# Optimization experiments

Measured on AMD Instinct MI355X. Metric: run time of the kernel, lower is better.

## Reference

```python
import jax, jax.numpy as jnp
import numpy as np

B, T, D = 8, 2048, 512
S = 4                 # n_slots
SLOT_DIM = D          # cfg.slot_dim defaults to d_model
SE = 8                # state_embed_dim
GH = 64               # gate_hidden
EMA = 0.99
SIGMA_FLOOR = 1e-3
OPEN2CLOSING, CLOSING2LOCKED, UNLOCK = 0.1, 0.03, 0.25
GAINS = jnp.array([1.0, 0.5, 0.1], dtype=jnp.float32)  # OPEN, CLOSING, LOCKED


def _glorot(k, shape, fi, fo):
    b = (6.0 / (fi + fo)) ** 0.5
    return jax.random.uniform(k, shape, jnp.float32, -b, b)


def setup_inputs() -> dict:
    key = jax.random.key(0)
    ks = jax.random.split(key, 8)
    gate_in = D + 1 + SE  # [h, z, state_embed]
    return {
        'h_seq': jax.random.normal(ks[0], (B, T, D), jnp.float32),
        'pred_W': _glorot(ks[1], (S, D, D), D, D),
        'pred_b': jnp.zeros((S, D), jnp.float32),
        'gate_W1': _glorot(ks[2], (S, gate_in, GH), gate_in, GH),
        'gate_b1': jnp.zeros((S, GH), jnp.float32),
        'gate_W2': _glorot(ks[3], (S, GH, 1), GH, 1),
        'gate_b2': jnp.zeros((S, 1), jnp.float32),
        'write_W': _glorot(ks[4], (S, D, SLOT_DIM), D, SLOT_DIM),
        'write_b': jnp.zeros((S, SLOT_DIM), jnp.float32),
        'w0': jnp.zeros((S, SLOT_DIM), jnp.float32),
        'state_embed': jax.random.normal(ks[5], (3, SE), jnp.float32),
    }


def reference(h_seq, pred_W, pred_b, gate_W1, gate_b1, gate_W2, gate_b2,
              write_W, write_b, w0, state_embed):
    Bb, Tt, Dd = h_seq.shape
    h_det = jax.lax.stop_gradient(h_seq)
    # per-slot next-step predictions (input detached, as in torch): (B,T,S,D)
    preds = jnp.einsum('btd,sdo->btso', h_det, pred_W) + pred_b
    # prediction emitted at t-1 targets h_t
    pred_prev = jnp.concatenate([jnp.zeros_like(preds[:, :1]), preds[:, :-1]], axis=1)
    valid = jnp.arange(Tt) > 0  # no surprise signal at t=0

    m0 = jnp.broadcast_to(w0, (Bb, S, SLOT_DIM)).astype(h_seq.dtype)
    carry0 = (m0,
              jnp.zeros((S,), jnp.float32),       # mu
              jnp.ones((S,), jnp.float32),        # sigma
              jnp.full((S,), 0.5, jnp.float32),   # gate_ema
              jnp.zeros((S,), jnp.int32))         # slot_state

    def step(carry, xs):
        m, mu, sigma, gate_ema, state = carry
        h_t, p_prev, ok = xs  # (B,D), (B,S,D), scalar bool
        # prediction-error surprise per slot
        err = jnp.sqrt(jnp.sum((p_prev - h_t[:, None, :]) ** 2, axis=-1) + 1e-8)  # (B,S)
        err = jnp.where(ok, err, 0.0)
        z = (err - mu) / jnp.maximum(sigma, SIGMA_FLOOR)  # (B,S)
        # gate MLP over [h, z, state_embed]
        se = state_embed[state]  # (S,SE)
        gin = jnp.concatenate([
            jnp.broadcast_to(h_t[:, None, :], (Bb, S, Dd)),
            z[..., None],
            jnp.broadcast_to(se[None], (Bb, S, SE))], axis=-1)
        hid = jax.nn.relu(jnp.einsum('bsi,sih->bsh', gin, gate_W1) + gate_b1)
        g = jax.nn.sigmoid(jnp.einsum('bsh,sho->bso', hid, gate_W2) + gate_b2)[..., 0]  # (B,S)
        # state-dependent write gain (OPEN/CLOSING/LOCKED)
        g_eff = g * GAINS[state]
        w_enc = jnp.einsum('bd,sdo->bso', h_t, write_W) + write_b
        m = (1.0 - g_eff[..., None]) * m + g_eff[..., None] * w_enc
        read = m.reshape(Bb, S * SLOT_DIM)
        # homeostatic bookkeeping (buffers: non-differentiable, EMA)
        err_s = jax.lax.stop_gradient(err)
        mu_n = jnp.where(ok, EMA * mu + (1 - EMA) * err_s.mean(0), mu)
        sigma_n = jnp.where(ok, EMA * sigma + (1 - EMA) * jnp.abs(err_s - mu).mean(0), sigma)
        gate_ema_n = EMA * gate_ema + (1 - EMA) * jax.lax.stop_gradient(g).mean(0)
        # state machine transitions on gate EMA
        st = jnp.where((state == 0) & (gate_ema_n < OPEN2CLOSING), 1, state)
        st = jnp.where((state == 1) & (gate_ema_n < CLOSING2LOCKED), 2,
             jnp.where((state == 1) & (gate_ema_n > UNLOCK), 0, st))
        st = jnp.where((state == 2) & (gate_ema_n > UNLOCK), 0, st)
        return (m, mu_n, sigma_n, gate_ema_n, st), read

    xs = (jnp.swapaxes(h_seq, 0, 1), jnp.swapaxes(pred_prev, 0, 1), valid)
    _, reads = jax.lax.scan(step, carry0, xs)
    return jnp.swapaxes(reads, 0, 1)  # (B,T,S*SLOT_DIM)
```

## Files before the change

### kernel.cpp

```cpp
#include <hip/hip_runtime.h>
#include <hip/hip_bf16.h>

#define Bb 8
#define Tt 2048
#define Dd 512
#define Ss 4
#define GHh 64
#define NCHUNK 64
#define CH 32

typedef __hip_bfloat16 bf16;
typedef short bf16x8 __attribute__((ext_vector_type(8)));
typedef float f32x4 __attribute__((ext_vector_type(4)));
__device__ __forceinline__ float b2f(bf16 x){ return __bfloat162float(x); }

#define GLOAD_LDS16(g, l) \
  __builtin_amdgcn_global_load_lds((const __attribute__((address_space(1))) unsigned int*)(const void*)(g), \
                                   (__attribute__((address_space(3))) unsigned int*)(l), 16, 0, 0)

__global__ __launch_bounds__(256) void k0a_cvt(const float* __restrict__ h, bf16* __restrict__ hb){
  int i = (blockIdx.x*256 + threadIdx.x)*4;
  float4 v = *reinterpret_cast<const float4*>(&h[i]);
  hb[i+0] = __float2bfloat16(v.x);
  hb[i+1] = __float2bfloat16(v.y);
  hb[i+2] = __float2bfloat16(v.z);
  hb[i+3] = __float2bfloat16(v.w);
}

__global__ __launch_bounds__(256) void k0b_pack(const float* __restrict__ predW,
    const float* __restrict__ writeW, const float* __restrict__ gateW1, bf16* __restrict__ Wt){
  __shared__ float tile[32][33];
  int k0 = blockIdx.x*32, n0 = blockIdx.y*32;
  int tx = threadIdx.x & 31, ty = threadIdx.x >> 5;
  #pragma unroll
  for (int p = 0; p < 4; ++p) {
    int kk = ty + p*8;
    int n = n0 + tx, k = k0 + kk;
    float v;
    if (n < 2048)      { int s=n>>9, o=n&511;              v = predW[((size_t)s*512+k)*512+o]; }
    else if (n < 4096) { int n2=n-2048; int s=n2>>9,o=n2&511; v = writeW[((size_t)s*512+k)*512+o]; }
    else               { int n2=n-4096; int s=n2>>6,hh=n2&63; v = gateW1[((size_t)s*521+k)*64+hh]; }
    tile[kk][tx] = v;
  }
  __syncthreads();
  #pragma unroll
  for (int p = 0; p < 4; ++p) {
    int nn = ty + p*8;
    Wt[(size_t)(n0+nn)*512 + k0 + tx] = __float2bfloat16(tile[tx][nn]);
  }
}

__global__ __launch_bounds__(256) void k1_mfma(
    const bf16* __restrict__ hb, const bf16* __restrict__ Wt,
    const float* __restrict__ h, const float* __restrict__ predb, const float* __restrict__ writeb,
    bf16* __restrict__ wenc, float* __restrict__ hg, float* __restrict__ errsq)
{
  __shared__ bf16 As[2][128*64];
  __shared__ bf16 Bs[2][128*64];
  const int tid = threadIdx.x;
  const int w = tid >> 6, lane = tid & 63;
  const int n0 = blockIdx.x * 128;
  const int row0 = blockIdx.y * 128;
  const int wm = w & 1, wn = w >> 1;
  const int mrow = lane & 15, kq = lane >> 4;

  f32x4 acc[4][4];
  #pragma unroll
  for (int i=0;i<4;++i)
    #pragma unroll
    for (int j=0;j<4;++j) acc[i][j] = (f32x4){0.f,0.f,0.f,0.f};

  const int srow  = lane >> 3;
  const int sslot = (lane & 7) ^ srow;
  const bf16* gaBase = hb + (size_t)(row0 + w*32 + srow)*512 + sslot*8;
  const bf16* gbBase = Wt + (size_t)(n0  + w*32 + srow)*512 + sslot*8;

  auto STAGE = [&](int buf, int kstep){
    const bf16* ga = gaBase + kstep*64;
    const bf16* gb = gbBase + kstep*64;
    bf16* lA = &As[buf][(w*32)*64];
    bf16* lB = &Bs[buf][(w*32)*64];
    #pragma unroll
    for (int i=0;i<4;++i) {
      GLOAD_LDS16(ga + (size_t)i*8*512, lA + i*8*64);
      GLOAD_LDS16(gb + (size_t)i*8*512, lB + i*8*64);
    }
  };

  auto COMPUTE = [&](int buf){
    #pragma unroll
    for (int kk=0; kk<2; ++kk) {
      bf16x8 af[4], bfr[4];
      #pragma unroll
      for (int mi=0;mi<4;++mi) {
        int r = wm*64 + mi*16 + mrow;
        af[mi] = *reinterpret_cast<const bf16x8*>(&As[buf][r*64 + (((kk*4+kq) ^ (r&7))<<3)]);
      }
      #pragma unroll
      for (int ni=0;ni<4;++ni) {
        int r = wn*64 + ni*16 + mrow;
        bfr[ni] = *reinterpret_cast<const bf16x8*>(&Bs[buf][r*64 + (((kk*4+kq) ^ (r&7))<<3)]);
      }
      #pragma unroll
      for (int mi=0;mi<4;++mi)
        #pragma unroll
        for (int ni=0;ni<4;++ni)
          acc[mi][ni] = __builtin_amdgcn_mfma_f32_16x16x32_bf16(af[mi], bfr[ni], acc[mi][ni], 0, 0, 0);
    }
  };

  STAGE(0, 0);
  __syncthreads();
  #pragma unroll
  for (int t = 0; t < 8; ++t) {
    if (t < 7) STAGE((t+1)&1, t+1);
    COMPUTE(t&1);
    __syncthreads();
  }

  if (n0 < 2048) {
    const int s = n0 >> 9;
    #pragma unroll
    for (int mi=0;mi<4;++mi) {
      #pragma unroll
      for (int reg=0;reg<4;++reg) {
        int r = row0 + wm*64 + mi*16 + kq*4 + reg;
        float sum = 0.f;
        if ((r & 2047) != 2047) {
          #pragma unroll
          for (int ni=0;ni<4;++ni) {
            int o = (n0 & 511) + wn*64 + ni*16 + mrow;
            float P = acc[mi][ni][reg] + predb[s*512 + o];
            float d = P - h[(size_t)(r+1)*512 + o];
            sum = fmaf(d, d, sum);
          }
        }
        #pragma unroll
        for (int off=1; off<16; off<<=1) sum += __shfl_xor(sum, off);
        if (mrow == 0 && (r & 2047) != 2047)
          atomicAdd(&errsq[(size_t)(r+1)*4 + s], sum);
      }
    }
  } else if (n0 < 4096) {
    #pragma unroll
    for (int mi=0;mi<4;++mi)
      #pragma unroll
      for (int ni=0;ni<4;++ni) {
        int n2 = n0 - 2048 + wn*64 + ni*16 + mrow;
        int s = n2 >> 9, o = n2 & 511;
        float wb = writeb[s*512 + o];
        #pragma unroll
        for (int reg=0;reg<4;++reg) {
          int r = row0 + wm*64 + mi*16 + kq*4 + reg;
          wenc[((size_t)r*4 + s)*512 + o] = __float2bfloat16(acc[mi][ni][reg] + wb);
        }
      }
  } else {
    #pragma unroll
    for (int mi=0;mi<4;++mi)
      #pragma unroll
      for (int ni=0;ni<4;++ni) {
        int n2 = n0 - 4096 + wn*64 + ni*16 + mrow;
        int s = n2 >> 6, hh = n2 & 63;
        #pragma unroll
        for (int reg=0;reg<4;++reg) {
          int r = row0 + wm*64 + mi*16 + kq*4 + reg;
          hg[((size_t)r*4 + s)*64 + hh] = acc[mi][ni][reg];
        }
      }
  }
}

__global__ void k2a_err(const float* __restrict__ errsq, float* __restrict__ err){
  int i = blockIdx.x*256 + threadIdx.x;
  int t = (i >> 2) & 2047;
  err[i] = (t > 0) ? sqrtf(errsq[i] + 1e-8f) : 0.f;
}

__global__ void k2b_em(const float* __restrict__ err, float* __restrict__ em){
  int i = blockIdx.x*256 + threadIdx.x;
  float sum = 0.f;
  #pragma unroll
  for (int b=0;b<8;++b) sum += err[b*8192 + i];
  em[i] = sum * 0.125f;
}

__global__ __launch_bounds__(256) void k2c_scan(const float* __restrict__ in, float* __restrict__ outv, float init){
  __shared__ float s_in[8192];
  __shared__ float sA[256], sB[256], s_entry[256];
  for (int i = threadIdx.x; i < 8192; i += 256) s_in[i] = in[i];
  __syncthreads();
  const int c = threadIdx.x >> 2, s = threadIdx.x & 3;
  float A = 1.f, B = 0.f;
  #pragma unroll 8
  for (int i = 0; i < 32; ++i) {
    int t = c*32 + i;
    if (t >= 1) { A *= 0.99f; B = fmaf(0.99f, B, 0.01f * s_in[t*4 + s]); }
  }
  sA[threadIdx.x] = A; sB[threadIdx.x] = B;
  __syncthreads();
  if (threadIdx.x < 4) {
    int ss = threadIdx.x;
    float v = init;
    for (int cc = 0; cc < 64; ++cc) {
      s_entry[cc*4 + ss] = v;
      v = fmaf(sA[cc*4 + ss], v, sB[cc*4 + ss]);
    }
  }
  __syncthreads();
  float v = s_entry[threadIdx.x];
  #pragma unroll 8
  for (int i = 0; i < 32; ++i) {
    int t = c*32 + i;
    outv[t*4 + s] = v;
    if (t >= 1) v = fmaf(0.99f, v, 0.01f * s_in[t*4 + s]);
  }
}

__global__ void k2d_sd(const float* __restrict__ err, const float* __restrict__ MU, float* __restrict__ sd){
  int i = blockIdx.x*256 + threadIdx.x;
  float mu = MU[i];
  float sum = 0.f;
  #pragma unroll
  for (int b=0;b<8;++b) sum += fabsf(err[b*8192 + i] - mu);
  sd[i] = sum * 0.125f;
}

__global__ void k2e_base(const float* __restrict__ gateW1, const float* __restrict__ semb,
                         const float* __restrict__ gateb1, float* __restrict__ base1){
  int i = blockIdx.x*256 + threadIdx.x;
  if (i < 768) {
    int hh = i & 63, k = (i >> 6) % 3, s = i / 192;
    float acc = gateb1[s*64 + hh];
    #pragma unroll
    for (int e = 0; e < 8; ++e)
      acc = fmaf(semb[k*8+e], gateW1[((size_t)s*521 + 513 + e)*64 + hh], acc);
    base1[i] = acc;
  }
}

__global__ void k3_gall(const float* __restrict__ hg, const float* __restrict__ err,
    const float* __restrict__ MU, const float* __restrict__ SIG,
    const float* __restrict__ gateW1, const float* __restrict__ base1,
    const float* __restrict__ gateW2, const float* __restrict__ gateb2,
    float* __restrict__ g_all)
{
  int i = blockIdx.x*256 + threadIdx.x;
  int k = i % 3;
  int bts = i / 3;
  int s = bts & 3;
  int t = (bts >> 2) & 2047;
  float e = err[bts];
  float z = (e - MU[t*4+s]) / fmaxf(SIG[t*4+s], 1e-3f);
  const float* hgp = &hg[(size_t)bts*64];
  const float* b1p = &base1[(s*3 + k)*64];
  const float* w1zp = &gateW1[((size_t)s*521 + 512)*64];
  const float* w2p = &gateW2[s*64];
  float logit = 0.f;
  for (int hh = 0; hh < 64; ++hh) {
    float hid = hgp[hh] + z*w1zp[hh] + b1p[hh];
    hid = fmaxf(hid, 0.f);
    logit = fmaf(hid, w2p[hh], logit);
  }
  logit += gateb2[s];
  g_all[i] = 1.f/(1.f + expf(-logit));
}

__global__ void k3b_gm(const float* __restrict__ g_all, float* __restrict__ gm){
  int i = blockIdx.x*256 + threadIdx.x;
  float sum = 0.f;
  #pragma unroll
  for (int b=0;b<8;++b) sum += g_all[((size_t)b*8192 + i/3)*3 + (i%3)];
  gm[i] = sum * 0.125f;
}

__global__ __launch_bounds__(256) void k4_scan(const float* __restrict__ gm, int* __restrict__ states){
  __shared__ float s_gm[2][6144];
  for (int i = threadIdx.x; i < 6144; i += 256) s_gm[0][i] = gm[i];
  __syncthreads();
  float ema = 0.5f; int st = 0;
  for (int c = 0; c < 4; ++c) {
    if (c < 3)
      for (int i = threadIdx.x; i < 6144; i += 256) s_gm[(c+1)&1][i] = gm[(c+1)*6144 + i];
    if (threadIdx.x < 4) {
      int s = threadIdx.x;
      const float* gp = &s_gm[c&1][s*3];
      int* sp = &states[c*2048 + s];
      #pragma unroll 8
      for (int tt = 0; tt < 512; ++tt) {
        sp[tt*4] = st;
        float g0 = gp[tt*12+0], g1 = gp[tt*12+1], g2 = gp[tt*12+2];
        float base = 0.99f * ema;
        float e0 = fmaf(0.01f, g0, base);
        float e1 = fmaf(0.01f, g1, base);
        float e2 = fmaf(0.01f, g2, base);
        ema = (st == 0) ? e0 : ((st == 1) ? e1 : e2);
        int n0 = (ema < 0.1f) ? 1 : 0;
        int n1 = (ema < 0.03f) ? 2 : ((ema > 0.25f) ? 0 : 1);
        int n2 = (ema > 0.25f) ? 0 : 2;
        st = (st == 0) ? n0 : ((st == 1) ? n1 : n2);
      }
    }
    __syncthreads();
  }
}

__global__ void k5_a(const float* __restrict__ g_all, const int* __restrict__ states, float* __restrict__ a){
  int i = blockIdx.x*256 + threadIdx.x;
  int ts = i & 8191;
  int st = states[ts];
  float gain = (st == 0) ? 1.f : ((st == 1) ? 0.5f : 0.1f);
  a[i] = g_all[(size_t)i*3 + st] * gain;
}

__global__ __launch_bounds__(64) void k6_pass1(const float* __restrict__ a, const bf16* __restrict__ wenc,
      float* __restrict__ q, float* __restrict__ Pc){
  int c = blockIdx.x, s = blockIdx.y, b = blockIdx.z;
  int d0 = threadIdx.x << 3;
  __shared__ float s_a[CH];
  if (threadIdx.x < CH) s_a[threadIdx.x] = a[(size_t)(b*2048 + c*CH + threadIdx.x)*4 + s];
  __syncthreads();
  float qv[8];
  #pragma unroll
  for (int j=0;j<8;++j) qv[j] = 0.f;
  float p = 1.f;
  const bf16* wp = &wenc[((size_t)(b*2048 + c*CH)*4 + s)*512 + d0];
  #pragma unroll 4
  for (int i = 0; i < CH; ++i) {
    float av = s_a[i];
    bf16x8 wv = *reinterpret_cast<const bf16x8*>(wp + (size_t)i*4*512);
    float om = 1.f - av;
    #pragma unroll
    for (int j=0;j<8;++j) qv[j] = fmaf(om, qv[j], av*b2f(((const bf16*)&wv)[j]));
    p *= om;
  }
  float* qp = &q[((size_t)(b*4+s)*NCHUNK + c)*512 + d0];
  #pragma unroll
  for (int j=0;j<8;++j) qp[j] = qv[j];
  if (threadIdx.x == 0) Pc[(b*4+s)*NCHUNK + c] = p;
}

__global__ __launch_bounds__(512) void k7_bound(const float* __restrict__ q, const float* __restrict__ Pc,
      const float* __restrict__ w0, float* __restrict__ m_start){
  int s = blockIdx.x, b = blockIdx.y, d = threadIdx.x;
  float m = w0[s*512 + d];
  for (int c = 0; c < NCHUNK; ++c) {
    m_start[((size_t)(b*4+s)*NCHUNK + c)*512 + d] = m;
    m = Pc[(b*4+s)*NCHUNK + c]*m + q[((size_t)(b*4+s)*NCHUNK + c)*512 + d];
  }
}

__global__ __launch_bounds__(64) void k8_pass2(const float* __restrict__ a, const bf16* __restrict__ wenc,
      const float* __restrict__ m_start, float* __restrict__ out){
  int c = blockIdx.x, s = blockIdx.y, b = blockIdx.z;
  int d0 = threadIdx.x << 3;
  __shared__ float s_a[CH];
  if (threadIdx.x < CH) s_a[threadIdx.x] = a[(size_t)(b*2048 + c*CH + threadIdx.x)*4 + s];
  __syncthreads();
  float m[8];
  const float* msp = &m_start[((size_t)(b*4+s)*NCHUNK + c)*512 + d0];
  #pragma unroll
  for (int j=0;j<8;++j) m[j] = msp[j];
  const bf16* wp = &wenc[((size_t)(b*2048 + c*CH)*4 + s)*512 + d0];
  float* op = &out[((size_t)(b*2048 + c*CH))*2048 + s*512 + d0];
  #pragma unroll 2
  for (int i = 0; i < CH; ++i) {
    float av = s_a[i];
    bf16x8 wv = *reinterpret_cast<const bf16x8*>(wp + (size_t)i*4*512);
    float om = 1.f - av;
    #pragma unroll
    for (int j=0;j<8;++j) m[j] = fmaf(om, m[j], av*b2f(((const bf16*)&wv)[j]));
    #pragma unroll
    for (int j=0;j<8;++j) op[(size_t)i*2048 + j] = m[j];
  }
}

extern "C" void kernel_launch(void* const* d_in, const int* in_sizes, int n_in,
                              void* d_out, int out_size, void* d_ws, size_t ws_size,
                              hipStream_t stream) {
  (void)in_sizes; (void)n_in; (void)out_size; (void)ws_size;
  const float* h      = (const float*)d_in[0];
  const float* predW  = (const float*)d_in[1];
  const float* predb  = (const float*)d_in[2];
  const float* gateW1 = (const float*)d_in[3];
  const float* gateb1 = (const float*)d_in[4];
  const float* gateW2 = (const float*)d_in[5];
  const float* gateb2 = (const float*)d_in[6];
  const float* writeW = (const float*)d_in[7];
  const float* writeb = (const float*)d_in[8];
  const float* w0     = (const float*)d_in[9];
  const float* semb   = (const float*)d_in[10];
  float* out = (float*)d_out;

  char* ws = (char*)d_ws;
  size_t off = 0;
  auto alloc = [&](size_t bytes) -> char* {
    char* p = ws + off; off += (bytes + 255) / 256 * 256; return p;
  };
  bf16*  wenc   = (bf16*) alloc((size_t)Bb*Tt*Ss*Dd*2);
  float* hg     = (float*)alloc((size_t)Bb*Tt*Ss*GHh*4);
  bf16*  hb     = (bf16*) alloc((size_t)Bb*Tt*Dd*2);
  bf16*  Wt     = (bf16*) alloc((size_t)4352*512*2);
  float* errsq  = (float*)alloc((size_t)Bb*Tt*Ss*4);
  float* err    = (float*)alloc((size_t)Bb*Tt*Ss*4);
  float* em     = (float*)alloc((size_t)Tt*Ss*4);
  float* MU     = (float*)alloc((size_t)Tt*Ss*4);
  float* sd     = (float*)alloc((size_t)Tt*Ss*4);
  float* SIG    = (float*)alloc((size_t)Tt*Ss*4);
  float* base1  = (float*)alloc((size_t)Ss*3*GHh*4);
  float* g_all  = (float*)alloc((size_t)Bb*Tt*Ss*3*4);
  float* gm     = (float*)alloc((size_t)Tt*Ss*3*4);
  int*   states = (int*)  alloc((size_t)Tt*Ss*4);
  float* av     = (float*)alloc((size_t)Bb*Tt*Ss*4);
  float* Pc     = (float*)alloc((size_t)Bb*Ss*NCHUNK*4);
  float* q      = (float*)alloc((size_t)Bb*Ss*NCHUNK*Dd*4);
  float* mst    = (float*)alloc((size_t)Bb*Ss*NCHUNK*Dd*4);

  hipMemsetAsync(errsq, 0, (size_t)Bb*Tt*Ss*4, stream);

  k0a_cvt<<<(Bb*Tt*Dd)/(256*4), 256, 0, stream>>>(h, hb);
  dim3 g0b(16, 136);
  k0b_pack<<<g0b, 256, 0, stream>>>(predW, writeW, gateW1, Wt);
  dim3 g1(34, 128);
  k1_mfma<<<g1, 256, 0, stream>>>(hb, Wt, h, predb, writeb, wenc, hg, errsq);
  k2a_err<<<(Bb*Tt*Ss)/256, 256, 0, stream>>>(errsq, err);
  k2b_em<<<(Tt*Ss)/256, 256, 0, stream>>>(err, em);
  k2c_scan<<<1, 256, 0, stream>>>(em, MU, 0.f);
  k2d_sd<<<(Tt*Ss)/256, 256, 0, stream>>>(err, MU, sd);
  k2c_scan<<<1, 256, 0, stream>>>(sd, SIG, 1.f);
  k2e_base<<<3, 256, 0, stream>>>(gateW1, semb, gateb1, base1);
  k3_gall<<<(Bb*Tt*Ss*3)/256, 256, 0, stream>>>(hg, err, MU, SIG, gateW1, base1, gateW2, gateb2, g_all);
  k3b_gm<<<(Tt*Ss*3)/256, 256, 0, stream>>>(g_all, gm);
  k4_scan<<<1, 256, 0, stream>>>(gm, states);
  k5_a<<<(Bb*Tt*Ss)/256, 256, 0, stream>>>(g_all, states, av);
  dim3 g6(NCHUNK, Ss, Bb);
  k6_pass1<<<g6, 64, 0, stream>>>(av, wenc, q, Pc);
  dim3 g7(Ss, Bb);
  k7_bound<<<g7, 512, 0, stream>>>(q, Pc, w0, mst);
  k8_pass2<<<g6, 64, 0, stream>>>(av, wenc, mst, out);
}
```

Baseline: 546.4 us.

## Remap GEMM blocks per XCD, fuse err kernels, vectorize gate and scan passes

The 1D GEMM grid is remapped so each group of eight consecutive block IDs is spread across interleaved work ranges, which is likely meant to keep neighbouring tiles on the same XCD and improve L2 reuse. The err and err-mean kernels are fused into one, saving a launch and a global round-trip. The gate MLP loop is unrolled with float4 loads. The chunked-scan passes switch to 4-wide contiguous lanes with float4 stores and a 128-thread boundary kernel, aiming for better coalescing of the large output writes. Together these touch several unrelated kernels.

```diff
diff --git a/kernel.cpp b/kernel.cpp
--- a/kernel.cpp
+++ b/kernel.cpp
@@ -11,8 +11,10 @@
 
 typedef __hip_bfloat16 bf16;
 typedef short bf16x8 __attribute__((ext_vector_type(8)));
+typedef short bf16x4 __attribute__((ext_vector_type(4)));
 typedef float f32x4 __attribute__((ext_vector_type(4)));
 __device__ __forceinline__ float b2f(bf16 x){ return __bfloat162float(x); }
+__device__ __forceinline__ float b2fs(short x){ bf16 t; __builtin_memcpy(&t,&x,2); return __bfloat162float(t); }
 
 #define GLOAD_LDS16(g, l) \
   __builtin_amdgcn_global_load_lds((const __attribute__((address_space(1))) unsigned int*)(const void*)(g), \
@@ -59,8 +61,10 @@
   __shared__ bf16 Bs[2][128*64];
   const int tid = threadIdx.x;
   const int w = tid >> 6, lane = tid & 63;
-  const int n0 = blockIdx.x * 128;
-  const int row0 = blockIdx.y * 128;
+  const int bid = blockIdx.x;
+  const int work = (bid & 7) * 544 + (bid >> 3);
+  const int n0   = (work % 34) * 128;
+  const int row0 = (work / 34) * 128;
   const int wm = w & 1, wn = w >> 1;
   const int mrow = lane & 15, kq = lane >> 4;
 
@@ -171,17 +175,16 @@
   }
 }
 
-__global__ void k2a_err(const float* __restrict__ errsq, float* __restrict__ err){
-  int i = blockIdx.x*256 + threadIdx.x;
-  int t = (i >> 2) & 2047;
-  err[i] = (t > 0) ? sqrtf(errsq[i] + 1e-8f) : 0.f;
-}
-
-__global__ void k2b_em(const float* __restrict__ err, float* __restrict__ em){
-  int i = blockIdx.x*256 + threadIdx.x;
+__global__ void k2ab(const float* __restrict__ errsq, float* __restrict__ err, float* __restrict__ em){
+  int i = blockIdx.x*256 + threadIdx.x;
+  int t = i >> 2;
   float sum = 0.f;
   #pragma unroll
-  for (int b=0;b<8;++b) sum += err[b*8192 + i];
+  for (int b=0;b<8;++b){
+    float e = (t > 0) ? sqrtf(errsq[b*8192 + i] + 1e-8f) : 0.f;
+    err[b*8192 + i] = e;
+    sum += e;
+  }
   em[i] = sum * 0.125f;
 }
 
@@ -252,15 +255,18 @@
   int t = (bts >> 2) & 2047;
   float e = err[bts];
   float z = (e - MU[t*4+s]) / fmaxf(SIG[t*4+s], 1e-3f);
-  const float* hgp = &hg[(size_t)bts*64];
-  const float* b1p = &base1[(s*3 + k)*64];
-  const float* w1zp = &gateW1[((size_t)s*521 + 512)*64];
-  const float* w2p = &gateW2[s*64];
+  const float4* hgp  = reinterpret_cast<const float4*>(&hg[(size_t)bts*64]);
+  const float4* b1p  = reinterpret_cast<const float4*>(&base1[(s*3 + k)*64]);
+  const float4* w1zp = reinterpret_cast<const float4*>(&gateW1[((size_t)s*521 + 512)*64]);
+  const float4* w2p  = reinterpret_cast<const float4*>(&gateW2[s*64]);
   float logit = 0.f;
-  for (int hh = 0; hh < 64; ++hh) {
-    float hid = hgp[hh] + z*w1zp[hh] + b1p[hh];
-    hid = fmaxf(hid, 0.f);
-    logit = fmaf(hid, w2p[hh], logit);
+  #pragma unroll
+  for (int hq = 0; hq < 16; ++hq) {
+    float4 hv = hgp[hq], bv = b1p[hq], wz = w1zp[hq], w2 = w2p[hq];
+    logit = fmaf(fmaxf(fmaf(z, wz.x, hv.x) + bv.x, 0.f), w2.x, logit);
+    logit = fmaf(fmaxf(fmaf(z, wz.y, hv.y) + bv.y, 0.f), w2.y, logit);
+    logit = fmaf(fmaxf(fmaf(z, wz.z, hv.z) + bv.z, 0.f), w2.z, logit);
+    logit = fmaf(fmaxf(fmaf(z, wz.w, hv.w) + bv.w, 0.f), w2.w, logit);
   }
   logit += gateb2[s];
   g_all[i] = 1.f/(1.f + expf(-logit));
@@ -316,7 +322,7 @@
 __global__ __launch_bounds__(64) void k6_pass1(const float* __restrict__ a, const bf16* __restrict__ wenc,
       float* __restrict__ q, float* __restrict__ Pc){
   int c = blockIdx.x, s = blockIdx.y, b = blockIdx.z;
-  int d0 = threadIdx.x << 3;
+  int d0 = threadIdx.x * 4;
   __shared__ float s_a[CH];
   if (threadIdx.x < CH) s_a[threadIdx.x] = a[(size_t)(b*2048 + c*CH + threadIdx.x)*4 + s];
   __syncthreads();
@@ -324,54 +330,68 @@
   #pragma unroll
   for (int j=0;j<8;++j) qv[j] = 0.f;
   float p = 1.f;
-  const bf16* wp = &wenc[((size_t)(b*2048 + c*CH)*4 + s)*512 + d0];
+  const bf16* wp = &wenc[((size_t)(b*2048 + c*CH)*4 + s)*512];
   #pragma unroll 4
   for (int i = 0; i < CH; ++i) {
     float av = s_a[i];
-    bf16x8 wv = *reinterpret_cast<const bf16x8*>(wp + (size_t)i*4*512);
     float om = 1.f - av;
-    #pragma unroll
-    for (int j=0;j<8;++j) qv[j] = fmaf(om, qv[j], av*b2f(((const bf16*)&wv)[j]));
+    bf16x4 w1 = *reinterpret_cast<const bf16x4*>(wp + (size_t)i*2048 + d0);
+    bf16x4 w2 = *reinterpret_cast<const bf16x4*>(wp + (size_t)i*2048 + 256 + d0);
+    #pragma unroll
+    for (int j=0;j<4;++j) qv[j]   = fmaf(om, qv[j],   av*b2fs(w1[j]));
+    #pragma unroll
+    for (int j=0;j<4;++j) qv[4+j] = fmaf(om, qv[4+j], av*b2fs(w2[j]));
     p *= om;
   }
-  float* qp = &q[((size_t)(b*4+s)*NCHUNK + c)*512 + d0];
-  #pragma unroll
-  for (int j=0;j<8;++j) qp[j] = qv[j];
+  float* qp = &q[((size_t)(b*4+s)*NCHUNK + c)*512];
+  *reinterpret_cast<float4*>(qp + d0)       = make_float4(qv[0],qv[1],qv[2],qv[3]);
+  *reinterpret_cast<float4*>(qp + 256 + d0) = make_float4(qv[4],qv[5],qv[6],qv[7]);
   if (threadIdx.x == 0) Pc[(b*4+s)*NCHUNK + c] = p;
 }
 
-__global__ __launch_bounds__(512) void k7_bound(const float* __restrict__ q, const float* __restrict__ Pc,
+__global__ __launch_bounds__(128) void k7_bound(const float* __restrict__ q, const float* __restrict__ Pc,
       const float* __restrict__ w0, float* __restrict__ m_start){
-  int s = blockIdx.x, b = blockIdx.y, d = threadIdx.x;
-  float m = w0[s*512 + d];
+  int s = blockIdx.x, b = blockIdx.y, d4 = threadIdx.x * 4;
+  float4 m = *reinterpret_cast<const float4*>(&w0[s*512 + d4]);
   for (int c = 0; c < NCHUNK; ++c) {
-    m_start[((size_t)(b*4+s)*NCHUNK + c)*512 + d] = m;
-    m = Pc[(b*4+s)*NCHUNK + c]*m + q[((size_t)(b*4+s)*NCHUNK + c)*512 + d];
+    *reinterpret_cast<float4*>(&m_start[((size_t)(b*4+s)*NCHUNK + c)*512 + d4]) = m;
+    float pc = Pc[(b*4+s)*NCHUNK + c];
+    float4 qv = *reinterpret_cast<const float4*>(&q[((size_t)(b*4+s)*NCHUNK + c)*512 + d4]);
+    m.x = fmaf(pc, m.x, qv.x);
+    m.y = fmaf(pc, m.y, qv.y);
+    m.z = fmaf(pc, m.z, qv.z);
+    m.w = fmaf(pc, m.w, qv.w);
   }
 }
 
 __global__ __launch_bounds__(64) void k8_pass2(const float* __restrict__ a, const bf16* __restrict__ wenc,
       const float* __restrict__ m_start, float* __restrict__ out){
   int c = blockIdx.x, s = blockIdx.y, b = blockIdx.z;
-  int d0 = threadIdx.x << 3;
+  int d0 = threadIdx.x * 4;
   __shared__ float s_a[CH];
   if (threadIdx.x < CH) s_a[threadIdx.x] = a[(size_t)(b*2048 + c*CH + threadIdx.x)*4 + s];
   __syncthreads();
-  float m[8];
-  const float* msp = &m_start[((size_t)(b*4+s)*NCHUNK + c)*512 + d0];
-  #pragma unroll
-  for (int j=0;j<8;++j) m[j] = msp[j];
-  const bf16* wp = &wenc[((size_t)(b*2048 + c*CH)*4 + s)*512 + d0];
-  float* op = &out[((size_t)(b*2048 + c*CH))*2048 + s*512 + d0];
+  const float* msp = &m_start[((size_t)(b*4+s)*NCHUNK + c)*512];
+  float4 m1 = *reinterpret_cast<const float4*>(msp + d0);
+  float4 m2 = *reinterpret_cast<const float4*>(msp + 256 + d0);
+  const bf16* wp = &wenc[((size_t)(b*2048 + c*CH)*4 + s)*512];
+  float* op = &out[((size_t)(b*2048 + c*CH))*2048 + s*512];
   #pragma unroll 2
   for (int i = 0; i < CH; ++i) {
     float av = s_a[i];
-    bf16x8 wv = *reinterpret_cast<const bf16x8*>(wp + (size_t)i*4*512);
     float om = 1.f - av;
-    #pragma unroll
-    for (int j=0;j<8;++j) m[j] = fmaf(om, m[j], av*b2f(((const bf16*)&wv)[j]));
-    #pragma unroll
-    for (int j=0;j<8;++j) op[(size_t)i*2048 + j] = m[j];
+    bf16x4 w1 = *reinterpret_cast<const bf16x4*>(wp + (size_t)i*2048 + d0);
+    bf16x4 w2 = *reinterpret_cast<const bf16x4*>(wp + (size_t)i*2048 + 256 + d0);
+    m1.x = fmaf(om, m1.x, av*b2fs(w1[0]));
+    m1.y = fmaf(om, m1.y, av*b2fs(w1[1]));
+    m1.z = fmaf(om, m1.z, av*b2fs(w1[2]));
+    m1.w = fmaf(om, m1.w, av*b2fs(w1[3]));
+    m2.x = fmaf(om, m2.x, av*b2fs(w2[0]));
+    m2.y = fmaf(om, m2.y, av*b2fs(w2[1]));
+    m2.z = fmaf(om, m2.z, av*b2fs(w2[2]));
+    m2.w = fmaf(om, m2.w, av*b2fs(w2[3]));
+    *reinterpret_cast<float4*>(op + (size_t)i*2048 + d0)       = m1;
+    *reinterpret_cast<float4*>(op + (size_t)i*2048 + 256 + d0) = m2;
   }
 }
 
@@ -421,10 +441,8 @@
   k0a_cvt<<<(Bb*Tt*Dd)/(256*4), 256, 0, stream>>>(h, hb);
   dim3 g0b(16, 136);
   k0b_pack<<<g0b, 256, 0, stream>>>(predW, writeW, gateW1, Wt);
-  dim3 g1(34, 128);
-  k1_mfma<<<g1, 256, 0, stream>>>(hb, Wt, h, predb, writeb, wenc, hg, errsq);
-  k2a_err<<<(Bb*Tt*Ss)/256, 256, 0, stream>>>(errsq, err);
-  k2b_em<<<(Tt*Ss)/256, 256, 0, stream>>>(err, em);
+  k1_mfma<<<4352, 256, 0, stream>>>(hb, Wt, h, predb, writeb, wenc, hg, errsq);
+  k2ab<<<(Tt*Ss)/256, 256, 0, stream>>>(errsq, err, em);
   k2c_scan<<<1, 256, 0, stream>>>(em, MU, 0.f);
   k2d_sd<<<(Tt*Ss)/256, 256, 0, stream>>>(err, MU, sd);
   k2c_scan<<<1, 256, 0, stream>>>(sd, SIG, 1.f);
@@ -436,6 +454,6 @@
   dim3 g6(NCHUNK, Ss, Bb);
   k6_pass1<<<g6, 64, 0, stream>>>(av, wenc, q, Pc);
   dim3 g7(Ss, Bb);
-  k7_bound<<<g7, 512, 0, stream>>>(q, Pc, w0, mst);
+  k7_bound<<<g7, 128, 0, stream>>>(q, Pc, w0, mst);
   k8_pass2<<<g6, 64, 0, stream>>>(av, wenc, mst, out);
 }
```

New measurement: 619.0 us. 13.3% more time.
